# Optimization experiments

Hardware: AMD Instinct MI355X
Metric: run time of the kernel (lower is better)

The kernel has to match this reference:

```python
import jax, jax.numpy as jnp
import numpy as np

N = 100_000   # nodes
E = 1_600_000 # edges
G = 64        # graphs in batch
IN_FEAT, H = 8, 16
NUM_CLASSES = 4


def _glorot(key, fi, fo):
    lim = float(np.sqrt(6.0 / (fi + fo)))
    return jax.random.uniform(key, (fi, fo), jnp.float32, -lim, lim)


def setup_inputs() -> dict:
    key = jax.random.key(0)
    ks = jax.random.split(key, 12)
    inp = {
        "x": jax.random.normal(ks[0], (N, IN_FEAT), jnp.float32),
        "edge_src": jax.random.randint(ks[1], (E,), 0, N, dtype=jnp.int32),
        "edge_dst": jax.random.randint(ks[2], (E,), 0, N, dtype=jnp.int32),
        "batch": jnp.sort(jax.random.randint(ks[3], (N,), 0, G, dtype=jnp.int32)),
    }
    dims = [(IN_FEAT, H), (H, 2 * H), (2 * H, 4 * H), (4 * H, 8 * H)]
    for i, (fi, fo) in enumerate(dims, 1):
        inp[f"W{i}"] = _glorot(ks[3 + i], fi, fo)
        inp[f"b{i}"] = jnp.zeros((fo,), jnp.float32)
    # PReLU slopes (torch default init 0.25, single parameter)
    inp["a1"] = jnp.float32(0.25)
    inp["a2"] = jnp.float32(0.25)
    inp["a3"] = jnp.float32(0.25)
    inp["Wlin"] = _glorot(ks[8], 8 * H, NUM_CLASSES)
    inp["blin"] = jnp.zeros((NUM_CLASSES,), jnp.float32)
    return inp


def _prelu(x, a):
    return jnp.where(x >= 0, x, a * x)


def reference(x, edge_src, edge_dst, batch,
              W1, b1, W2, b2, W3, b3, W4, b4,
              a1, a2, a3, Wlin, blin):
    # GCNConv: add self-loops, symmetric normalization D^-1/2 A_hat D^-1/2
    loops = jnp.arange(N, dtype=edge_src.dtype)
    src = jnp.concatenate([edge_src, loops])  # [E+N]
    dst = jnp.concatenate([edge_dst, loops])
    deg = jax.ops.segment_sum(jnp.ones_like(src, jnp.float32), dst, num_segments=N)
    dinv = jax.lax.rsqrt(jnp.maximum(deg, 1.0))
    norm = dinv[src] * dinv[dst]  # [E+N]

    def gcn(h, W, b):
        h = h @ W                                   # [N, Fout]
        msg = h[src] * norm[:, None]                # gather + edge scale
        return jax.ops.segment_sum(msg, dst, num_segments=N) + b

    h = _prelu(gcn(x, W1, b1), a1)
    h = _prelu(gcn(h, W2, b2), a2)
    h = _prelu(gcn(h, W3, b3), a3)
    h = gcn(h, W4, b4)

    # global mean pool over graphs
    sums = jax.ops.segment_sum(h, batch, num_segments=G)          # [G, 8H]
    cnts = jax.ops.segment_sum(jnp.ones((N,), jnp.float32), batch, num_segments=G)
    pooled = sums / jnp.maximum(cnts, 1.0)[:, None]
    # dropout(p=0.25) is identity at inference
    return pooled @ Wlin + blin                                    # [G, 4]
```

## Files before the change

kernel.cpp:

```cpp
#include <hip/hip_runtime.h>
#include <hip/hip_fp16.h>

#define NN 100000
#define NE 1600000
#define NG 64

#define BSHIFT 7
#define BUCKW (1 << BSHIFT)
#define NBUCK ((NN + BUCKW - 1) >> BSHIFT)
#define BCAP 2560
#define BIN_CHUNK 4096

union H8 { float4 f4; __half2 h2[4]; };
__device__ __forceinline__ void h8_to_f(const H8& h, float* f) {
    float2 a = __half22float2(h.h2[0]);
    float2 b = __half22float2(h.h2[1]);
    float2 c = __half22float2(h.h2[2]);
    float2 d = __half22float2(h.h2[3]);
    f[0]=a.x; f[1]=a.y; f[2]=b.x; f[3]=b.y; f[4]=c.x; f[5]=c.y; f[6]=d.x; f[7]=d.y;
}
__device__ __forceinline__ H8 f_to_h8(const float* f) {
    H8 h;
    h.h2[0] = __floats2half2_rn(f[0], f[1]);
    h.h2[1] = __floats2half2_rn(f[2], f[3]);
    h.h2[2] = __floats2half2_rn(f[4], f[5]);
    h.h2[3] = __floats2half2_rn(f[6], f[7]);
    return h;
}
__device__ __forceinline__ float prelu_f(float x, float s) {
    return fmaxf(x, 0.f) + s * fminf(x, 0.f);
}

__global__ __launch_bounds__(256) void bin_kernel(const int* __restrict__ src,
                                                  const int* __restrict__ dst,
                                                  int* __restrict__ bcnt,
                                                  unsigned* __restrict__ binned, int E) {
    __shared__ int h[NBUCK];
    __shared__ int cur[NBUCK];
    for (int i = threadIdx.x; i < NBUCK; i += 256) h[i] = 0;
    __syncthreads();
    int base = blockIdx.x * BIN_CHUNK;
    int end = base + BIN_CHUNK; if (end > E) end = E;
    for (int e = base + threadIdx.x; e < end; e += 256)
        atomicAdd(&h[dst[e] >> BSHIFT], 1);
    __syncthreads();
    for (int i = threadIdx.x; i < NBUCK; i += 256) {
        int c = h[i];
        cur[i] = c ? (i * BCAP + atomicAdd(&bcnt[i], c)) : 0;
    }
    __syncthreads();
    for (int e = base + threadIdx.x; e < end; e += 256) {
        unsigned s = (unsigned)src[e], d = (unsigned)dst[e];
        int pos = atomicAdd(&cur[d >> BSHIFT], 1);
        binned[pos] = (s << BSHIFT) | (d & (BUCKW - 1));
    }
}

__global__ __launch_bounds__(256) void build_csr_kernel(
    const unsigned* __restrict__ binned, const int* __restrict__ bucket_cnt,
    int* __restrict__ deg, float* __restrict__ dinv,
    int* __restrict__ roff, int* __restrict__ csr_src, int n) {
    __shared__ int ldeg[BUCKW];
    __shared__ int lscan[2][BUCKW];
    __shared__ int lcur[BUCKW];
    int b = blockIdx.x;
    int tid = threadIdx.x;
    for (int i = tid; i < BUCKW; i += 256) ldeg[i] = 0;
    __syncthreads();
    int start = b * BCAP, cnt = bucket_cnt[b];
    for (int k = tid; k < cnt; k += 256)
        atomicAdd(&ldeg[binned[start + k] & (BUCKW - 1)], 1);
    __syncthreads();
    if (tid < BUCKW) lscan[0][tid] = ldeg[tid];
    __syncthreads();
    int cur = 0;
    for (int off = 1; off < BUCKW; off <<= 1) {
        int x = 0;
        if (tid < BUCKW) {
            x = lscan[cur][tid];
            if (tid >= off) x += lscan[cur][tid - off];
        }
        __syncthreads();
        if (tid < BUCKW) lscan[cur ^ 1][tid] = x;
        __syncthreads();
        cur ^= 1;
    }
    int v0 = b << BSHIFT;
    if (tid < BUCKW) {
        int v = v0 + tid;
        if (v < n) {
            int dg = ldeg[tid];
            deg[v] = dg;
            dinv[v] = rsqrtf((float)dg + 1.0f);
            int r = start + lscan[cur][tid] - dg;
            roff[v] = r;
            lcur[tid] = r;
        }
    }
    __syncthreads();
    for (int k = tid; k < cnt; k += 256) {
        unsigned e = binned[start + k];
        int pos = atomicAdd(&lcur[e & (BUCKW - 1)], 1);
        csr_src[pos] = (int)(e >> BSHIFT);
    }
}

__global__ __launch_bounds__(256) void makeM_kernel(
    const float* __restrict__ W4, const float* __restrict__ b4,
    const float* __restrict__ Wlin, const float* __restrict__ blin,
    float* __restrict__ M, float* __restrict__ bb) {
    int t = threadIdx.x;
    int k = t >> 2, c = t & 3;
    float m = 0.f;
    for (int j = 0; j < 128; ++j) m += W4[k * 128 + j] * Wlin[j * 4 + c];
    M[k * 4 + c] = m;
    if (t < 4) {
        float v = blin[t];
        for (int j = 0; j < 128; ++j) v += b4[j] * Wlin[j * 4 + t];
        bb[t] = v;
    }
}

__global__ __launch_bounds__(256) void aggmm1_kernel(
    const float* __restrict__ x, const int* __restrict__ row_off,
    const int* __restrict__ deg, const float* __restrict__ dinv,
    const int* __restrict__ csr_src, const float* __restrict__ W1,
    const float* __restrict__ b1, const float* __restrict__ a1,
    float4* __restrict__ Aout, int n) {
    __shared__ float Wl[8 * 16];
    for (int i = threadIdx.x; i < 8 * 16; i += 256) Wl[i] = W1[i];
    __syncthreads();
    int idx = blockIdx.x * 256 + threadIdx.x;
    if (idx >= n * 2) return;
    int v = idx >> 1;
    int c = idx & 1;
    const float4* h4 = (const float4*)x;
    float dvv = dinv[v];
    float4 self = h4[(size_t)v * 2 + c];
    float4 acc = make_float4(self.x * dvv, self.y * dvv, self.z * dvv, self.w * dvv);
    int start = row_off[v], cnt = deg[v];
    const int* __restrict__ row = csr_src + start;
    int j = 0;
    for (; j + 4 <= cnt; j += 4) {
        int s0 = row[j], s1 = row[j + 1], s2 = row[j + 2], s3 = row[j + 3];
        float d0 = dinv[s0], d1 = dinv[s1], d2 = dinv[s2], d3 = dinv[s3];
        float4 a0 = h4[(size_t)s0 * 2 + c];
        float4 a1v = h4[(size_t)s1 * 2 + c];
        float4 a2 = h4[(size_t)s2 * 2 + c];
        float4 a3 = h4[(size_t)s3 * 2 + c];
        acc.x += (a0.x * d0 + a1v.x * d1) + (a2.x * d2 + a3.x * d3);
        acc.y += (a0.y * d0 + a1v.y * d1) + (a2.y * d2 + a3.y * d3);
        acc.z += (a0.z * d0 + a1v.z * d1) + (a2.z * d2 + a3.z * d3);
        acc.w += (a0.w * d0 + a1v.w * d1) + (a2.w * d2 + a3.w * d3);
    }
    for (; j < cnt; ++j) {
        int s = row[j];
        float ds = dinv[s];
        float4 a = h4[(size_t)s * 2 + c];
        acc.x += a.x * ds; acc.y += a.y * ds; acc.z += a.z * ds; acc.w += a.w * ds;
    }
    float t[4] = { acc.x * dvv, acc.y * dvv, acc.z * dvv, acc.w * dvv };
    float po[4];
#pragma unroll
    for (int k = 0; k < 4; ++k) po[k] = __shfl_xor(t[k], 1, 64);
    int ob = c * 8;
    int e0 = c * 4, e1 = 4 - e0;
    float accm[8];
#pragma unroll
    for (int q = 0; q < 8; ++q) accm[q] = b1[ob + q];
#pragma unroll
    for (int k = 0; k < 4; ++k) {
        float r1 = t[k], r2 = po[k];
        const float* w1 = &Wl[(e0 + k) * 16 + ob];
        const float* w2 = &Wl[(e1 + k) * 16 + ob];
#pragma unroll
        for (int q = 0; q < 8; ++q) accm[q] += r1 * w1[q] + r2 * w2[q];
    }
    float s = *a1;
    float o[8];
#pragma unroll
    for (int q = 0; q < 8; ++q) o[q] = prelu_f(accm[q], s) * dvv;
    H8 h = f_to_h8(o);
    Aout[(size_t)v * 2 + c] = h.f4;
}

__global__ __launch_bounds__(256) void aggmm2_kernel(
    const float4* __restrict__ hs, const int* __restrict__ row_off,
    const int* __restrict__ deg, const float* __restrict__ dinv,
    const int* __restrict__ csr_src, const float* __restrict__ W2,
    const float* __restrict__ b2, const float* __restrict__ a2,
    float4* __restrict__ Aout, int n) {
    __shared__ float Wl[16 * 32];
    for (int i = threadIdx.x; i < 16 * 32; i += 256) Wl[i] = W2[i];
    __syncthreads();
    int idx = blockIdx.x * 256 + threadIdx.x;
    if (idx >= n * 2) return;
    int v = idx >> 1;
    int c = idx & 1;
    float a[8];
    { H8 h; h.f4 = hs[(size_t)v * 2 + c]; h8_to_f(h, a); }
    int start = row_off[v], cnt = deg[v];
    const int* __restrict__ row = csr_src + start;
    int j = 0;
    for (; j + 8 <= cnt; j += 8) {
        H8 hh[8];
#pragma unroll
        for (int q = 0; q < 8; ++q) hh[q].f4 = hs[(size_t)row[j + q] * 2 + c];
#pragma unroll
        for (int q = 0; q < 8; ++q) {
            float f[8]; h8_to_f(hh[q], f);
#pragma unroll
            for (int k = 0; k < 8; ++k) a[k] += f[k];
        }
    }
    for (; j < cnt; ++j) {
        H8 h; h.f4 = hs[(size_t)row[j] * 2 + c];
        float f[8]; h8_to_f(h, f);
#pragma unroll
        for (int k = 0; k < 8; ++k) a[k] += f[k];
    }
    float dvv = dinv[v];
#pragma unroll
    for (int k = 0; k < 8; ++k) a[k] *= dvv;
    float pa[8];
#pragma unroll
    for (int k = 0; k < 8; ++k) pa[k] = __shfl_xor(a[k], 1, 64);
    int ob = c * 16;
    int e0 = c * 8, e1 = 8 - e0;
    float accm[16];
#pragma unroll
    for (int q = 0; q < 16; ++q) accm[q] = b2[ob + q];
#pragma unroll
    for (int k = 0; k < 8; ++k) {
        float r1 = a[k], r2 = pa[k];
        const float* w1 = &Wl[(e0 + k) * 32 + ob];
        const float* w2 = &Wl[(e1 + k) * 32 + ob];
#pragma unroll
        for (int q = 0; q < 16; ++q) accm[q] += r1 * w1[q] + r2 * w2[q];
    }
    float s = *a2;
    float o[16];
#pragma unroll
    for (int q = 0; q < 16; ++q) o[q] = prelu_f(accm[q], s) * dvv;
    H8 h0 = f_to_h8(o);
    H8 h1 = f_to_h8(o + 8);
    Aout[(size_t)v * 4 + c * 2 + 0] = h0.f4;
    Aout[(size_t)v * 4 + c * 2 + 1] = h1.f4;
}

__global__ __launch_bounds__(256) void aggmm3_kernel(
    const float4* __restrict__ hs, const int* __restrict__ row_off,
    const int* __restrict__ deg, const float* __restrict__ dinv,
    const int* __restrict__ csr_src, const float* __restrict__ W3,
    const float* __restrict__ b3, const float* __restrict__ a3,
    const float* __restrict__ M, float4* __restrict__ z, int n) {
    __shared__ float Wl[32 * 64];
    __shared__ float Ml[64 * 4];
    for (int i = threadIdx.x; i < 32 * 64; i += 256) Wl[i] = W3[i];
    for (int i = threadIdx.x; i < 64 * 4; i += 256) Ml[i] = M[i];
    __syncthreads();
    int idx = blockIdx.x * 256 + threadIdx.x;
    if (idx >= n * 4) return;
    int v = idx >> 2;
    int c = idx & 3;
    float a[8];
    { H8 h; h.f4 = hs[(size_t)v * 4 + c]; h8_to_f(h, a); }
    int start = row_off[v], cnt = deg[v];
    const int* __restrict__ row = csr_src + start;
    int j = 0;
    for (; j + 8 <= cnt; j += 8) {
        H8 hh[8];
#pragma unroll
        for (int q = 0; q < 8; ++q) hh[q].f4 = hs[(size_t)row[j + q] * 4 + c];
#pragma unroll
        for (int q = 0; q < 8; ++q) {
            float f[8]; h8_to_f(hh[q], f);
#pragma unroll
            for (int k = 0; k < 8; ++k) a[k] += f[k];
        }
    }
    for (; j < cnt; ++j) {
        H8 h; h.f4 = hs[(size_t)row[j] * 4 + c];
        float f[8]; h8_to_f(h, f);
#pragma unroll
        for (int k = 0; k < 8; ++k) a[k] += f[k];
    }
    float dvv = dinv[v];
#pragma unroll
    for (int k = 0; k < 8; ++k) a[k] *= dvv;
    int ob = c * 16;
    float accm[16];
#pragma unroll
    for (int q = 0; q < 16; ++q) accm[q] = b3[ob + q];
#pragma unroll
    for (int m = 0; m < 4; ++m) {
        float cur[8];
        if (m == 0) {
#pragma unroll
            for (int k = 0; k < 8; ++k) cur[k] = a[k];
        } else {
#pragma unroll
            for (int k = 0; k < 8; ++k) cur[k] = __shfl_xor(a[k], m, 64);
        }
        int eb = (c ^ m) * 8;
#pragma unroll
        for (int k = 0; k < 8; ++k) {
            float rk = cur[k];
            const float* wp = &Wl[(eb + k) * 64 + ob];
#pragma unroll
            for (int q = 0; q < 16; ++q) accm[q] += rk * wp[q];
        }
    }
    float s = *a3;
    float px = 0.f, py = 0.f, pz = 0.f, pw = 0.f;
#pragma unroll
    for (int q = 0; q < 16; ++q) {
        float o = prelu_f(accm[q], s) * dvv;
        const float* mp = &Ml[(ob + q) * 4];
        px += o * mp[0]; py += o * mp[1]; pz += o * mp[2]; pw += o * mp[3];
    }
#pragma unroll
    for (int mask = 1; mask <= 2; mask <<= 1) {
        px += __shfl_xor(px, mask, 64);
        py += __shfl_xor(py, mask, 64);
        pz += __shfl_xor(pz, mask, 64);
        pw += __shfl_xor(pw, mask, 64);
    }
    if (c == 0) z[v] = make_float4(px, py, pz, pw);
}

__global__ __launch_bounds__(256) void aggpool4_kernel(
    const float4* __restrict__ z, const int* __restrict__ row_off,
    const int* __restrict__ deg, const float* __restrict__ dinv,
    const int* __restrict__ csr_src, const int* __restrict__ batch,
    float* __restrict__ sums, float* __restrict__ cnt, int n) {
    __shared__ float lacc[NG * 4];
    __shared__ float lcnt[NG];
    int tid = threadIdx.x;
    if (tid < NG * 4) lacc[tid] = 0.f;
    if (tid < NG) lcnt[tid] = 0.f;
    __syncthreads();
    int v = blockIdx.x * 256 + tid;
    bool valid = (v < n);
    float cx = 0.f, cy = 0.f, cz = 0.f, cw = 0.f, rc = 0.f;
    int g = -1;
    if (valid) {
        float4 acc = z[v];
        int start = row_off[v], dcnt = deg[v];
        const int* __restrict__ row = csr_src + start;
        int j = 0;
        for (; j + 4 <= dcnt; j += 4) {
            float4 a0 = z[row[j]];
            float4 a1 = z[row[j + 1]];
            float4 a2 = z[row[j + 2]];
            float4 a3 = z[row[j + 3]];
            acc.x += (a0.x + a1.x) + (a2.x + a3.x);
            acc.y += (a0.y + a1.y) + (a2.y + a3.y);
            acc.z += (a0.z + a1.z) + (a2.z + a3.z);
            acc.w += (a0.w + a1.w) + (a2.w + a3.w);
        }
        for (; j < dcnt; ++j) {
            float4 a = z[row[j]];
            acc.x += a.x; acc.y += a.y; acc.z += a.z; acc.w += a.w;
        }
        float dv = dinv[v];
        cx = acc.x * dv; cy = acc.y * dv; cz = acc.z * dv; cw = acc.w * dv;
        rc = 1.f;
        g = batch[v];
    }
    int g0 = __shfl(g, 0, 64);
    if (__all(g == g0 || !valid)) {
#pragma unroll
        for (int mask = 32; mask >= 1; mask >>= 1) {
            cx += __shfl_xor(cx, mask, 64);
            cy += __shfl_xor(cy, mask, 64);
            cz += __shfl_xor(cz, mask, 64);
            cw += __shfl_xor(cw, mask, 64);
            rc += __shfl_xor(rc, mask, 64);
        }
        if ((tid & 63) == 0) {
            float* lp = &lacc[g0 * 4];
            atomicAdd(lp + 0, cx); atomicAdd(lp + 1, cy);
            atomicAdd(lp + 2, cz); atomicAdd(lp + 3, cw);
            atomicAdd(&lcnt[g0], rc);
        }
    } else if (valid) {
        float* lp = &lacc[g * 4];
        atomicAdd(lp + 0, cx); atomicAdd(lp + 1, cy);
        atomicAdd(lp + 2, cz); atomicAdd(lp + 3, cw);
        atomicAdd(&lcnt[g], 1.f);
    }
    __syncthreads();
    if (tid < NG * 4) {
        float val = lacc[tid];
        if (val != 0.f) atomicAdd(&sums[tid], val);
    }
    if (tid < NG) {
        float val = lcnt[tid];
        if (val != 0.f) atomicAdd(&cnt[tid], val);
    }
}

__global__ void head_kernel(const float* __restrict__ sums, const float* __restrict__ cnt,
                            const float* __restrict__ bb, float* __restrict__ out) {
    int t = threadIdx.x;
    int g = t >> 2, c = t & 3;
    out[t] = sums[t] / fmaxf(cnt[g], 1.f) + bb[c];
}

extern "C" void kernel_launch(void* const* d_in, const int* in_sizes, int n_in,
                              void* d_out, int out_size, void* d_ws, size_t ws_size,
                              hipStream_t stream) {
    const float* x    = (const float*)d_in[0];
    const int* esrc   = (const int*)d_in[1];
    const int* edst   = (const int*)d_in[2];
    const int* batch  = (const int*)d_in[3];
    const float* W1 = (const float*)d_in[4],  *b1 = (const float*)d_in[5];
    const float* W2 = (const float*)d_in[6],  *b2 = (const float*)d_in[7];
    const float* W3 = (const float*)d_in[8],  *b3 = (const float*)d_in[9];
    const float* W4 = (const float*)d_in[10], *b4 = (const float*)d_in[11];
    const float* a1 = (const float*)d_in[12];
    const float* a2 = (const float*)d_in[13];
    const float* a3 = (const float*)d_in[14];
    const float* Wlin = (const float*)d_in[15], *blin = (const float*)d_in[16];
    float* out = (float*)d_out;

    const int N = NN, E = NE;
    const int NBIN = (E + BIN_CHUNK - 1) / BIN_CHUNK;

    char* w = (char*)d_ws;
    size_t off = 0;
    auto alloc = [&](size_t bytes) { size_t r = off; off += (bytes + 255) & ~(size_t)255; return r; };
    size_t o_bcnt = alloc((size_t)NBUCK * 4);
    size_t o_pool = alloc((size_t)NG * 4 * 4);
    size_t o_cnt  = alloc((size_t)NG * 4);
    size_t zero_bytes = off;
    size_t o_deg  = alloc((size_t)N * 4);
    size_t o_dinv = alloc((size_t)N * 4);
    size_t o_roff = alloc((size_t)N * 4);
    size_t o_csrc = alloc((size_t)NBUCK * BCAP * 4);
    size_t o_bin  = alloc((size_t)NBUCK * BCAP * 4);
    size_t o_A1   = alloc((size_t)N * 16 * 2);
    size_t o_A2   = alloc((size_t)N * 32 * 2);
    size_t o_z    = alloc((size_t)N * 4 * 4);
    size_t o_M    = alloc((size_t)64 * 4 * 4);
    size_t o_bb   = alloc((size_t)4 * 4);
    (void)ws_size;
    int*      bcnt   = (int*)(w + o_bcnt);
    float*    pool   = (float*)(w + o_pool);
    float*    cnt    = (float*)(w + o_cnt);
    int*      deg    = (int*)(w + o_deg);
    float*    dinv   = (float*)(w + o_dinv);
    int*      roff   = (int*)(w + o_roff);
    int*      csrc   = (int*)(w + o_csrc);
    unsigned* binned = (unsigned*)(w + o_bin);
    float4*   A1     = (float4*)(w + o_A1);
    float4*   A2     = (float4*)(w + o_A2);
    float4*   z      = (float4*)(w + o_z);
    float*    M      = (float*)(w + o_M);
    float*    bb     = (float*)(w + o_bb);

    hipMemsetAsync(w, 0, zero_bytes, stream);

    makeM_kernel<<<1, 256, 0, stream>>>(W4, b4, Wlin, blin, M, bb);

    bin_kernel<<<NBIN, 256, 0, stream>>>(esrc, edst, bcnt, binned, E);
    build_csr_kernel<<<NBUCK, 256, 0, stream>>>(binned, bcnt, deg, dinv, roff, csrc, N);

    aggmm1_kernel<<<(N * 2 + 255) / 256, 256, 0, stream>>>(
        x, roff, deg, dinv, csrc, W1, b1, a1, A1, N);

    aggmm2_kernel<<<(N * 2 + 255) / 256, 256, 0, stream>>>(
        A1, roff, deg, dinv, csrc, W2, b2, a2, A2, N);

    aggmm3_kernel<<<(N * 4 + 255) / 256, 256, 0, stream>>>(
        A2, roff, deg, dinv, csrc, W3, b3, a3, M, z, N);

    aggpool4_kernel<<<(N + 255) / 256, 256, 0, stream>>>(
        z, roff, deg, dinv, csrc, batch, pool, cnt, N);
    head_kernel<<<1, 256, 0, stream>>>(pool, cnt, bb, out);
}
```

Before: 237.8 us.

## Use coarse 1024-node buckets for edge binning, refine to 128-node CSR buckets

Edge binning now sorts edges into 98 coarse buckets of 1024 destinations instead of 782 fine buckets. This shrinks the shared histograms and cuts the number of global atomics on bucket counters. Each CSR-build block then scans its parent coarse bucket and keeps only the edges of its 128-node sub-bucket, so every binned edge is read 8 times in each pass. The bin kernel also halves its chunk size and keeps src/dst in registers, so edges are loaded once rather than twice. Coarse-bucket capacity is fixed at 18432, which is a risk if degree skew overflows a bucket.

```diff
diff --git a/kernel.cpp b/kernel.cpp
--- a/kernel.cpp
+++ b/kernel.cpp
@@ -5,11 +5,17 @@
 #define NE 1600000
 #define NG 64
 
-#define BSHIFT 7
-#define BUCKW (1 << BSHIFT)
-#define NBUCK ((NN + BUCKW - 1) >> BSHIFT)
-#define BCAP 2560
-#define BIN_CHUNK 4096
+#define BSHIFT_F 7
+#define BUCKW_F (1 << BSHIFT_F)
+#define NBUCK_F ((NN + BUCKW_F - 1) >> BSHIFT_F)
+#define BCAP_F 2560
+
+#define BSHIFT_C 10
+#define BUCKW_C (1 << BSHIFT_C)
+#define NBUCK_C ((NN + BUCKW_C - 1) >> BSHIFT_C)
+#define BCAP_C 18432
+
+#define BIN_CHUNK 2048
 
 union H8 { float4 f4; __half2 h2[4]; };
 __device__ __forceinline__ void h8_to_f(const H8& h, float* f) {
@@ -35,24 +41,38 @@
                                                   const int* __restrict__ dst,
                                                   int* __restrict__ bcnt,
                                                   unsigned* __restrict__ binned, int E) {
-    __shared__ int h[NBUCK];
-    __shared__ int cur[NBUCK];
-    for (int i = threadIdx.x; i < NBUCK; i += 256) h[i] = 0;
+    __shared__ int h[NBUCK_C];
+    __shared__ int cur[NBUCK_C];
+    int tid = threadIdx.x;
+    for (int i = tid; i < NBUCK_C; i += 256) h[i] = 0;
     __syncthreads();
     int base = blockIdx.x * BIN_CHUNK;
     int end = base + BIN_CHUNK; if (end > E) end = E;
-    for (int e = base + threadIdx.x; e < end; e += 256)
-        atomicAdd(&h[dst[e] >> BSHIFT], 1);
-    __syncthreads();
-    for (int i = threadIdx.x; i < NBUCK; i += 256) {
+    int ms[8], md[8];
+#pragma unroll
+    for (int k = 0; k < 8; ++k) {
+        int e = base + k * 256 + tid;
+        if (e < end) { ms[k] = src[e]; md[k] = dst[e]; }
+    }
+#pragma unroll
+    for (int k = 0; k < 8; ++k) {
+        int e = base + k * 256 + tid;
+        if (e < end) atomicAdd(&h[md[k] >> BSHIFT_C], 1);
+    }
+    __syncthreads();
+    for (int i = tid; i < NBUCK_C; i += 256) {
         int c = h[i];
-        cur[i] = c ? (i * BCAP + atomicAdd(&bcnt[i], c)) : 0;
-    }
-    __syncthreads();
-    for (int e = base + threadIdx.x; e < end; e += 256) {
-        unsigned s = (unsigned)src[e], d = (unsigned)dst[e];
-        int pos = atomicAdd(&cur[d >> BSHIFT], 1);
-        binned[pos] = (s << BSHIFT) | (d & (BUCKW - 1));
+        cur[i] = c ? (i * BCAP_C + atomicAdd(&bcnt[i], c)) : 0;
+    }
+    __syncthreads();
+#pragma unroll
+    for (int k = 0; k < 8; ++k) {
+        int e = base + k * 256 + tid;
+        if (e < end) {
+            unsigned s = (unsigned)ms[k], d = (unsigned)md[k];
+            int pos = atomicAdd(&cur[d >> BSHIFT_C], 1);
+            binned[pos] = (s << BSHIFT_C) | (d & (BUCKW_C - 1));
+        }
     }
 }
 
@@ -60,48 +80,57 @@
     const unsigned* __restrict__ binned, const int* __restrict__ bucket_cnt,
     int* __restrict__ deg, float* __restrict__ dinv,
     int* __restrict__ roff, int* __restrict__ csr_src, int n) {
-    __shared__ int ldeg[BUCKW];
-    __shared__ int lscan[2][BUCKW];
-    __shared__ int lcur[BUCKW];
+    __shared__ int ldeg[BUCKW_F];
+    __shared__ int lscan[2][BUCKW_F];
+    __shared__ int lcur[BUCKW_F];
     int b = blockIdx.x;
     int tid = threadIdx.x;
-    for (int i = tid; i < BUCKW; i += 256) ldeg[i] = 0;
-    __syncthreads();
-    int start = b * BCAP, cnt = bucket_cnt[b];
-    for (int k = tid; k < cnt; k += 256)
-        atomicAdd(&ldeg[binned[start + k] & (BUCKW - 1)], 1);
-    __syncthreads();
-    if (tid < BUCKW) lscan[0][tid] = ldeg[tid];
+    int cb = b >> 3;
+    unsigned sub = (unsigned)(b & 7);
+    for (int i = tid; i < BUCKW_F; i += 256) ldeg[i] = 0;
+    __syncthreads();
+    int start_c = cb * BCAP_C, cntc = bucket_cnt[cb];
+    for (int k = tid; k < cntc; k += 256) {
+        unsigned e = binned[start_c + k];
+        unsigned dlow = e & (BUCKW_C - 1);
+        if ((dlow >> BSHIFT_F) == sub) atomicAdd(&ldeg[dlow & (BUCKW_F - 1)], 1);
+    }
+    __syncthreads();
+    if (tid < BUCKW_F) lscan[0][tid] = ldeg[tid];
     __syncthreads();
     int cur = 0;
-    for (int off = 1; off < BUCKW; off <<= 1) {
+    for (int off = 1; off < BUCKW_F; off <<= 1) {
         int x = 0;
-        if (tid < BUCKW) {
+        if (tid < BUCKW_F) {
             x = lscan[cur][tid];
             if (tid >= off) x += lscan[cur][tid - off];
         }
         __syncthreads();
-        if (tid < BUCKW) lscan[cur ^ 1][tid] = x;
+        if (tid < BUCKW_F) lscan[cur ^ 1][tid] = x;
         __syncthreads();
         cur ^= 1;
     }
-    int v0 = b << BSHIFT;
-    if (tid < BUCKW) {
+    int v0 = b << BSHIFT_F;
+    int start_f = b * BCAP_F;
+    if (tid < BUCKW_F) {
         int v = v0 + tid;
         if (v < n) {
             int dg = ldeg[tid];
             deg[v] = dg;
             dinv[v] = rsqrtf((float)dg + 1.0f);
-            int r = start + lscan[cur][tid] - dg;
+            int r = start_f + lscan[cur][tid] - dg;
             roff[v] = r;
             lcur[tid] = r;
         }
     }
     __syncthreads();
-    for (int k = tid; k < cnt; k += 256) {
-        unsigned e = binned[start + k];
-        int pos = atomicAdd(&lcur[e & (BUCKW - 1)], 1);
-        csr_src[pos] = (int)(e >> BSHIFT);
+    for (int k = tid; k < cntc; k += 256) {
+        unsigned e = binned[start_c + k];
+        unsigned dlow = e & (BUCKW_C - 1);
+        if ((dlow >> BSHIFT_F) == sub) {
+            int pos = atomicAdd(&lcur[dlow & (BUCKW_F - 1)], 1);
+            csr_src[pos] = (int)(e >> BSHIFT_C);
+        }
     }
 }
 
@@ -431,15 +460,15 @@
     char* w = (char*)d_ws;
     size_t off = 0;
     auto alloc = [&](size_t bytes) { size_t r = off; off += (bytes + 255) & ~(size_t)255; return r; };
-    size_t o_bcnt = alloc((size_t)NBUCK * 4);
+    size_t o_bcnt = alloc((size_t)NBUCK_C * 4);
     size_t o_pool = alloc((size_t)NG * 4 * 4);
     size_t o_cnt  = alloc((size_t)NG * 4);
     size_t zero_bytes = off;
     size_t o_deg  = alloc((size_t)N * 4);
     size_t o_dinv = alloc((size_t)N * 4);
     size_t o_roff = alloc((size_t)N * 4);
-    size_t o_csrc = alloc((size_t)NBUCK * BCAP * 4);
-    size_t o_bin  = alloc((size_t)NBUCK * BCAP * 4);
+    size_t o_csrc = alloc((size_t)NBUCK_F * BCAP_F * 4);
+    size_t o_bin  = alloc((size_t)NBUCK_C * BCAP_C * 4);
     size_t o_A1   = alloc((size_t)N * 16 * 2);
     size_t o_A2   = alloc((size_t)N * 32 * 2);
     size_t o_z    = alloc((size_t)N * 4 * 4);
@@ -465,7 +494,7 @@
     makeM_kernel<<<1, 256, 0, stream>>>(W4, b4, Wlin, blin, M, bb);
 
     bin_kernel<<<NBIN, 256, 0, stream>>>(esrc, edst, bcnt, binned, E);
-    build_csr_kernel<<<NBUCK, 256, 0, stream>>>(binned, bcnt, deg, dinv, roff, csrc, N);
+    build_csr_kernel<<<NBUCK_F, 256, 0, stream>>>(binned, bcnt, deg, dinv, roff, csrc, N);
 
     aggmm1_kernel<<<(N * 2 + 255) / 256, 256, 0, stream>>>(
         x, roff, deg, dinv, csrc, W1, b1, a1, A1, N);
```

Result: slower. 269.7 us (+13.4%).
